# Optimization experiments

Hardware: AMD Instinct MI355X
Metric: run time of the kernel (lower is better)

The kernel has to match this reference:

```python
import jax, jax.numpy as jnp
import numpy as np

NPOINT = 1024   # number of sampled centers
NSAMPLE = 32    # neighbors per center
BN_EPS = 1e-5


def setup_inputs() -> dict:
    key = jax.random.key(0)
    ks = jax.random.split(key, 6)
    B, N, C = 8, 4096, 6
    inp = {
        "xyz": jax.random.normal(ks[0], (B, N, 3), jnp.float32),
        "points": jax.random.normal(ks[1], (B, N, C), jnp.float32),
        "W0": jax.random.normal(ks[2], (64, 9), jnp.float32) * 0.1,
        "g0": jnp.ones((64,), jnp.float32),
        "b0": jnp.zeros((64,), jnp.float32),
        "W1": jax.random.normal(ks[3], (64, 64), jnp.float32) * 0.1,
        "g1": jnp.ones((64,), jnp.float32),
        "b1": jnp.zeros((64,), jnp.float32),
        "W2": jax.random.normal(ks[4], (128, 64), jnp.float32) * 0.1,
        "g2": jnp.ones((128,), jnp.float32),
        "b2": jnp.zeros((128,), jnp.float32),
    }
    return inp


def sample_and_group(xyz, points):
    # xyz: [B,N,3], points: [B,N,C]
    B, N, _ = xyz.shape
    stride = N // NPOINT
    new_xyz = xyz[:, ::stride]                      # [B,S,3] deterministic subsample (FPS surrogate)
    # squared pairwise distances via ||a||^2 + ||b||^2 - 2 a.b  -> [B,S,N]
    d = (jnp.sum(new_xyz * new_xyz, -1)[:, :, None]
         + jnp.sum(xyz * xyz, -1)[:, None, :]
         - 2.0 * jnp.einsum('bsd,bnd->bsn', new_xyz, xyz))
    _, idx = jax.lax.top_k(-d, NSAMPLE)             # [B,S,K] KNN indices
    gather = jax.vmap(lambda arr, i: arr[i])        # per-batch gather: [N,C],[S,K] -> [S,K,C]
    g_xyz = gather(xyz, idx) - new_xyz[:, :, None, :]   # relative coords [B,S,K,3]
    g_pts = gather(points, idx)                     # [B,S,K,C]
    new_points = jnp.concatenate([g_xyz, g_pts], -1)    # [B,S,K,3+C]
    return new_xyz, new_points


def mlp_layer(x, W, g, b):
    # Conv2d(1x1, bias=False) == channel contraction; BN2d with batch stats; ReLU
    x = jnp.einsum('bskc,oc->bsko', x, W)
    m = jnp.mean(x, axis=(0, 1, 2))
    v = jnp.var(x, axis=(0, 1, 2))
    x = (x - m) * jax.lax.rsqrt(v + BN_EPS) * g + b
    return jax.nn.relu(x)


def reference(xyz, points, W0, g0, b0, W1, g1, b1, W2, g2, b2):
    new_xyz, x = sample_and_group(xyz, points)      # x: [B,S,K,9]
    x = mlp_layer(x, W0, g0, b0)
    x = mlp_layer(x, W1, g1, b1)
    x = mlp_layer(x, W2, g2, b2)
    new_points = jnp.max(x, axis=2)                 # max-pool over neighbor dim K -> [B,S,128]
    return new_xyz, new_points
```

## Files before the change

kernel.cpp:

```cpp
#include <hip/hip_runtime.h>
#include <float.h>
#include <stdint.h>

#define TOT   262144
#define NPTS  4096
#define KNN   32
#define BN_EPS 1e-5f
#define CAPV  64
#define TILEP 2048

typedef _Float16 f16;
typedef _Float16 f16x2 __attribute__((ext_vector_type(2)));
typedef _Float16 f16x4 __attribute__((ext_vector_type(4)));
typedef _Float16 f16x8 __attribute__((ext_vector_type(8)));
typedef float    f32x4 __attribute__((ext_vector_type(4)));

__device__ __forceinline__ int mbcnt64(unsigned long long m){
  return __builtin_amdgcn_mbcnt_hi((unsigned)(m>>32),
         __builtin_amdgcn_mbcnt_lo((unsigned)(m & 0xffffffffull), 0));
}
__device__ __forceinline__ unsigned f2ord(float f){
  unsigned u = __float_as_uint(f);
  return u ^ (((unsigned)((int)u >> 31)) | 0x80000000u);
}
__device__ __forceinline__ f16x2 bnrelu2(f16x2 x, f16x2 a, f16x2 c){
  f16x2 r = x*a + c;
  const f16 z = (f16)0.f;
  r[0] = r[0] > z ? r[0] : z;
  r[1] = r[1] > z ? r[1] : z;
  return r;
}
__device__ __forceinline__ void writeElem(int n, int e, float qx, float qy, float qz,
    const float* __restrict__ xb3, const float* __restrict__ fb,
    f16* __restrict__ grouped, f16* __restrict__ g16){
  float px = xb3[n*3+0], py = xb3[n*3+1], pz = xb3[n*3+2];
  f16 a[16];
  a[0]=(f16)(px-qx); a[1]=(f16)(py-qy); a[2]=(f16)(pz-qz);
  #pragma unroll
  for (int c6=0;c6<6;c6++) a[3+c6] = (f16)fb[n*6+c6];
  #pragma unroll
  for (int i=9;i<16;i++) a[i]=(f16)0.f;
  #pragma unroll
  for (int c=0;c<9;c++) grouped[c*TOT+e] = a[c];
  f16x8 lo, hi;
  #pragma unroll
  for (int i=0;i<8;i++){ lo[i]=a[i]; hi[i]=a[8+i]; }
  *(f16x8*)(g16 + (size_t)e*16)     = lo;
  *(f16x8*)(g16 + (size_t)e*16 + 8) = hi;
}

__global__ __launch_bounds__(256) void knn_gather(
    const float* __restrict__ xyz, const float* __restrict__ pts,
    f16* __restrict__ grouped, f16* __restrict__ g16,
    float* __restrict__ out_newxyz){
  __shared__ float4 tile[TILEP];
  __shared__ unsigned wk[8][CAPV];
  __shared__ unsigned short wi[8][CAPV];
  __shared__ unsigned lcnt[8];
  const int tid = threadIdx.x, lane = tid & 63, wv = tid >> 6;
  const int q0 = blockIdx.x*8 + wv*2;
  const int b  = (blockIdx.x*8) >> 10;
  const float* xb3 = xyz + (size_t)b*NPTS*3;
  float qx[2],qy[2],qz[2],qq[2];
  #pragma unroll
  for (int t=0;t<2;t++){
    int n = ((q0+t) & 1023)*4;
    qx[t]=xb3[n*3+0]; qy[t]=xb3[n*3+1]; qz[t]=xb3[n*3+2];
    qq[t]=qx[t]*qx[t]+qy[t]*qy[t]+qz[t]*qz[t];
  }
  if (tid < 8) lcnt[tid] = 0;
  if (lane == 0){
    #pragma unroll
    for (int t=0;t<2;t++){
      out_newxyz[(q0+t)*3+0]=qx[t]; out_newxyz[(q0+t)*3+1]=qy[t];
      out_newxyz[(q0+t)*3+2]=qz[t];
    }
  }

  float dmin[2] = {FLT_MAX, FLT_MAX};
  #pragma unroll 1
  for (int r=0; r<2; ++r){
    __syncthreads();
    #pragma unroll
    for (int k=0;k<8;k++){
      int p = r*TILEP + k*256 + tid;
      float x = xb3[p*3+0], y = xb3[p*3+1], z = xb3[p*3+2];
      tile[k*256+tid] = make_float4(x,y,z, x*x+y*y+z*z);
    }
    __syncthreads();
    #pragma unroll 4
    for (int i=0;i<32;i++){
      float4 P = tile[i*64+lane];
      #pragma unroll
      for (int t=0;t<2;t++){
        float d = (qq[t]+P.w) - 2.f*(qx[t]*P.x+qy[t]*P.y+qz[t]*P.z);
        dmin[t] = d < dmin[t] ? d : dmin[t];
      }
    }
  }
  float sm[2] = {dmin[0], dmin[1]};
  #pragma unroll
  for (int k=2;k<=64;k<<=1){
    #pragma unroll
    for (int j=k>>1;j>0;j>>=1){
      bool keepmin = (((lane&k)==0) == ((lane&j)==0));
      #pragma unroll
      for (int t=0;t<2;t++){
        float o = __shfl_xor(sm[t], j, 64);
        sm[t] = keepmin ? fminf(sm[t],o) : fmaxf(sm[t],o);
      }
    }
  }
  float Uf[2];
  #pragma unroll
  for (int t=0;t<2;t++) Uf[t] = __shfl(sm[t], 31, 64);

  #pragma unroll 1
  for (int r=0; r<2; ++r){
    __syncthreads();
    #pragma unroll
    for (int k=0;k<8;k++){
      int p = r*TILEP + k*256 + tid;
      float x = xb3[p*3+0], y = xb3[p*3+1], z = xb3[p*3+2];
      tile[k*256+tid] = make_float4(x,y,z, x*x+y*y+z*z);
    }
    __syncthreads();
    #pragma unroll 2
    for (int i=0;i<32;i++){
      float4 P = tile[i*64+lane];
      #pragma unroll
      for (int t=0;t<2;t++){
        float d = (qq[t]+P.w) - 2.f*(qx[t]*P.x+qy[t]*P.y+qz[t]*P.z);
        if (d <= Uf[t]){
          unsigned p2 = atomicAdd(&lcnt[wv*2+t], 1u);
          if (p2 < CAPV){
            wk[wv*2+t][p2] = f2ord(d);
            wi[wv*2+t][p2] = (unsigned short)(r*TILEP + i*64 + lane);
          }
        }
      }
    }
  }
  int cnt[2] = {(int)lcnt[wv*2], (int)lcnt[wv*2+1]};

  unsigned long long v[2];
  #pragma unroll
  for (int t=0;t<2;t++){
    unsigned myk = (lane<cnt[t]) ? wk[wv*2+t][lane] : 0xFFFFFFFFu;
    unsigned myi = (lane<cnt[t]) ? wi[wv*2+t][lane] : 0u;
    v[t] = (((unsigned long long)myk)<<16) | myi;
  }
  #pragma unroll
  for (int k=2;k<=64;k<<=1){
    #pragma unroll
    for (int j=k>>1;j>0;j>>=1){
      bool keepmin = (((lane&k)==0) == ((lane&j)==0));
      #pragma unroll
      for (int t=0;t<2;t++){
        unsigned long long o = __shfl_xor(v[t], j, 64);
        v[t] = keepmin ? (v[t]<o?v[t]:o) : (v[t]>o?v[t]:o);
      }
    }
  }

  const float* fb = pts + (size_t)b*NPTS*6;
  #pragma unroll 1
  for (int t=0;t<2;t++){
    const int ebase = (q0+t)*KNN;
    if (cnt[t] <= CAPV){
      if (lane < KNN){
        int n = (int)(v[t] & 0xffffull);
        writeElem(n, ebase+lane, qx[t],qy[t],qz[t], xb3, fb, grouped, g16);
      }
    } else {
      unsigned V=0;
      for (int bit=31; bit>=0; --bit){
        unsigned X = V | (1u<<bit);
        int c=0;
        for (int j=0;j<64;j++){
          int n = j*64+lane;
          float px=xb3[n*3], py=xb3[n*3+1], pz=xb3[n*3+2];
          float d = qq[t] + (px*px+py*py+pz*pz)
                  - 2.f*(qx[t]*px+qy[t]*py+qz[t]*pz);
          c += __popcll(__ballot(f2ord(d) < X));
        }
        if (c < KNN) V = X;
      }
      int cnt2=0;
      for (int pass=0; pass<2; ++pass){
        for (int j=0;j<64;j++){
          int n = j*64+lane;
          float px=xb3[n*3], py=xb3[n*3+1], pz=xb3[n*3+2];
          float d = qq[t] + (px*px+py*py+pz*pz)
                  - 2.f*(qx[t]*px+qy[t]*py+qz[t]*pz);
          unsigned kk = f2ord(d);
          bool sel = pass ? (kk==V) : (kk<V);
          unsigned long long msk = __ballot(sel);
          int pos = cnt2 + mbcnt64(msk);
          if (sel && pos < KNN)
            writeElem(n, ebase+pos, qx[t],qy[t],qz[t], xb3, fb, grouped, g16);
          cnt2 += __popcll(msk);
        }
      }
    }
  }
}

__global__ __launch_bounds__(256) void stats0m(const f16* __restrict__ grouped,
    float* __restrict__ s0m){
  const int lane = threadIdx.x & 63, wv = threadIdx.x >> 6;
  const int c = lane & 15, q = lane >> 4;
  const int base = (blockIdx.x*4 + wv)*512;
  f16x8 cfill = {};
  if (c == 9){
    #pragma unroll
    for (int i=0;i<8;i++) cfill[i] = (f16)1.f;
  }
  f32x4 acc = {0.f,0.f,0.f,0.f};
  #pragma unroll 4
  for (int chunk=0; chunk<16; ++chunk){
    int e = base + chunk*32 + q*8;
    f16x8 f = cfill;
    if (c < 9) f = *(const f16x8*)(grouped + (size_t)c*TOT + e);
    acc = __builtin_amdgcn_mfma_f32_16x16x32_f16(f, f, acc, 0,0,0);
  }
  __shared__ float red[4][16][16];
  #pragma unroll
  for (int i=0;i<4;i++) red[wv][q*4+i][c] = acc[i];
  __syncthreads();
  const int tid = threadIdx.x;
  if (tid < 160){
    int row = tid>>4, col = tid&15;
    float vv = red[0][row][col]+red[1][row][col]+red[2][row][col]+red[3][row][col];
    atomicAdd(&s0m[tid], vv);
  }
}

__device__ __forceinline__ void bn0_coeffs(int tid, const float* __restrict__ s0m,
    const float* __restrict__ W0, const float* __restrict__ g0,
    const float* __restrict__ b0, float* __restrict__ A0s,
    float* __restrict__ ac0c, float* __restrict__ Ssh){
  if (tid < 160) Ssh[tid] = s0m[tid];
  __syncthreads();
  if (tid < 64){
    float w[9];
    #pragma unroll
    for (int c=0;c<9;c++) w[c]=W0[tid*9+c];
    const float inv = 1.f/(float)TOT;
    float m=0.f;
    #pragma unroll
    for (int c=0;c<9;c++) m = fmaf(w[c], Ssh[c*16+9], m);
    m *= inv;
    float e2=0.f;
    #pragma unroll
    for (int c1=0;c1<9;c1++){
      float t=0.f;
      #pragma unroll
      for (int c2=0;c2<9;c2++) t = fmaf(w[c2], Ssh[c1*16+c2], t);
      e2 = fmaf(w[c1], t, e2);
    }
    e2 *= inv;
    float var = e2 - m*m;
    float a = g0[tid]*rsqrtf(var + BN_EPS);
    A0s[tid]  = a;
    ac0c[tid] = fmaf(-m, a, b0[tid]);
  }
  __syncthreads();
}

__global__ __launch_bounds__(256, 2) void layer1s(
    const f16* __restrict__ g16, const float* __restrict__ s0m,
    const float* __restrict__ W0, const float* __restrict__ g0,
    const float* __restrict__ b0, const float* __restrict__ W1,
    float* __restrict__ s1g){
  __shared__ f16 sW0[2048];
  __shared__ f16 sW1[4096];
  __shared__ float ac0c[64];
  __shared__ float A0s[64];
  __shared__ float Ssh[160];
  __shared__ f16 hb0[4][16][72];
  __shared__ float sred[4][128];
  const int tid = threadIdx.x;
  const int lane = tid & 63, wv = tid >> 6;
  const int e16 = lane & 15, q = lane >> 4;
  bn0_coeffs(tid, s0m, W0, g0, b0, A0s, ac0c, Ssh);
  #pragma unroll
  for (int idx=tid; idx<2048; idx+=256){
    int o = idx>>5, c = idx&31;
    sW0[idx] = (f16)(c<9 ? A0s[o]*W0[o*9+c] : 0.f);
  }
  #pragma unroll
  for (int idx=tid; idx<4096; idx+=256) sW1[idx] = (f16)W1[idx];
  __syncthreads();

  const int base = blockIdx.x*256 + wv*64;
  float ssum[16], ssq[16];
  #pragma unroll
  for (int i=0;i<16;i++){ ssum[i]=0.f; ssq[i]=0.f; }

  #pragma unroll 1
  for (int sub=0; sub<4; ++sub){
    int elem = base + sub*16 + e16;
    f16x8 bg = {};
    if (q < 2) bg = *(const f16x8*)(g16 + (size_t)elem*16 + q*8);
    #pragma unroll
    for (int m=0;m<4;m++){
      f32x4 acc = *(const f32x4*)(&ac0c[m*16 + q*4]);
      f16x8 A0f = *(const f16x8*)(&sW0[(m*16+e16)*32 + q*8]);
      acc = __builtin_amdgcn_mfma_f32_16x16x32_f16(A0f, bg, acc, 0,0,0);
      f16x4 w;
      w[0]=(f16)fmaxf(acc[0],0.f); w[1]=(f16)fmaxf(acc[1],0.f);
      w[2]=(f16)fmaxf(acc[2],0.f); w[3]=(f16)fmaxf(acc[3],0.f);
      *(f16x4*)(&hb0[wv][e16][m*16 + q*4]) = w;
    }
    f32x4 acc2[4];
    #pragma unroll
    for (int m=0;m<4;m++) acc2[m] = (f32x4){0.f,0.f,0.f,0.f};
    #pragma unroll
    for (int s=0;s<2;s++){
      f16x8 bh = *(const f16x8*)(&hb0[wv][e16][s*32 + q*8]);
      #pragma unroll
      for (int m=0;m<4;m++){
        f16x8 A1f = *(const f16x8*)(&sW1[(m*16+e16)*64 + s*32 + q*8]);
        acc2[m] = __builtin_amdgcn_mfma_f32_16x16x32_f16(A1f, bh, acc2[m], 0,0,0);
      }
    }
    #pragma unroll
    for (int m=0;m<4;m++)
      #pragma unroll
      for (int i=0;i<4;i++){
        float x = acc2[m][i];
        ssum[m*4+i] += x;
        ssq[m*4+i]  = fmaf(x, x, ssq[m*4+i]);
      }
  }
  #pragma unroll
  for (int t=0;t<16;t++){
    float a = ssum[t], bq = ssq[t];
    #pragma unroll
    for (int off=1; off<16; off<<=1){
      a  += __shfl_xor(a,  off, 64);
      bq += __shfl_xor(bq, off, 64);
    }
    ssum[t]=a; ssq[t]=bq;
  }
  if (e16==0){
    #pragma unroll
    for (int m=0;m<4;m++)
      #pragma unroll
      for (int i=0;i<4;i++){
        int ch = m*16 + q*4 + i;
        sred[wv][ch]    = ssum[m*4+i];
        sred[wv][64+ch] = ssq[m*4+i];
      }
  }
  __syncthreads();
  if (tid < 128){
    float v = sred[0][tid]+sred[1][tid]+sred[2][tid]+sred[3][tid];
    atomicAdd(&s1g[tid], v);
  }
}

__global__ __launch_bounds__(256, 2) void layer2max(
    const f16* __restrict__ g16, const float* __restrict__ s0m,
    const float* __restrict__ W0, const float* __restrict__ g0,
    const float* __restrict__ b0, const float* __restrict__ W1,
    const float* __restrict__ W2, const float* __restrict__ s1g,
    const float* __restrict__ g1, const float* __restrict__ b1,
    float* __restrict__ maxbuf, float* __restrict__ s2g){
  __shared__ f16 sW0[2048];
  __shared__ f16 sW1[4096];
  __shared__ float ac0c[64];
  __shared__ float A0s[64];
  __shared__ float Ssh[160];
  __shared__ f16 ac1s[128];
  __shared__ f16 hb0[4][16][72];
  __shared__ f16 hb1[4][2][16][72];
  float (*redbuf)[256] = (float(*)[256])hb0;
  const int tid = threadIdx.x;
  const int lane = tid & 63, wv = tid >> 6;
  const int e16 = lane & 15, q = lane >> 4;
  bn0_coeffs(tid, s0m, W0, g0, b0, A0s, ac0c, Ssh);
  #pragma unroll
  for (int idx=tid; idx<2048; idx+=256){
    int o = idx>>5, c = idx&31;
    sW0[idx] = (f16)(c<9 ? A0s[o]*W0[o*9+c] : 0.f);
  }
  #pragma unroll
  for (int idx=tid; idx<4096; idx+=256) sW1[idx] = (f16)W1[idx];
  if (tid < 64){
    const float inv = 1.f/(float)TOT;
    float m = s1g[tid]*inv;
    float vv = s1g[64+tid]*inv - m*m;
    float a = g1[tid]*rsqrtf(vv + BN_EPS);
    ac1s[tid]    = (f16)a;
    ac1s[64+tid] = (f16)fmaf(-m, a, b1[tid]);
  }
  __syncthreads();

  f16x8 Bw[8][2];
  #pragma unroll
  for (int nt=0;nt<8;nt++)
    #pragma unroll
    for (int s=0;s<2;s++){
      const float* src = W2 + (nt*16+e16)*64 + s*32 + q*8;
      f16x8 f;
      #pragma unroll
      for (int j=0;j<8;j++) f[j] = (f16)src[j];
      Bw[nt][s] = f;
    }

  float ssum[8], ssq[8];
  #pragma unroll
  for (int i=0;i<8;i++){ ssum[i]=0.f; ssq[i]=0.f; }

  #pragma unroll 1
  for (int qq=0; qq<2; ++qq){
    const int qid = blockIdx.x*8 + wv*2 + qq;
    #pragma unroll 1
    for (int mt=0; mt<2; ++mt){
      int elem = qid*32 + mt*16 + e16;
      f16x8 bg = {};
      if (q < 2) bg = *(const f16x8*)(g16 + (size_t)elem*16 + q*8);
      #pragma unroll
      for (int m=0;m<4;m++){
        f32x4 acc = *(const f32x4*)(&ac0c[m*16 + q*4]);
        f16x8 A0f = *(const f16x8*)(&sW0[(m*16+e16)*32 + q*8]);
        acc = __builtin_amdgcn_mfma_f32_16x16x32_f16(A0f, bg, acc, 0,0,0);
        f16x4 w;
        w[0]=(f16)fmaxf(acc[0],0.f); w[1]=(f16)fmaxf(acc[1],0.f);
        w[2]=(f16)fmaxf(acc[2],0.f); w[3]=(f16)fmaxf(acc[3],0.f);
        *(f16x4*)(&hb0[wv][e16][m*16 + q*4]) = w;
      }
      f32x4 acc2[4];
      #pragma unroll
      for (int m=0;m<4;m++) acc2[m] = (f32x4){0.f,0.f,0.f,0.f};
      #pragma unroll
      for (int s=0;s<2;s++){
        f16x8 bh = *(const f16x8*)(&hb0[wv][e16][s*32 + q*8]);
        #pragma unroll
        for (int m=0;m<4;m++){
          f16x8 A1f = *(const f16x8*)(&sW1[(m*16+e16)*64 + s*32 + q*8]);
          acc2[m] = __builtin_amdgcn_mfma_f32_16x16x32_f16(A1f, bh, acc2[m], 0,0,0);
        }
      }
      #pragma unroll
      for (int m=0;m<4;m++){
        f16x4 a4 = *(const f16x4*)(&ac1s[m*16 + q*4]);
        f16x4 c4 = *(const f16x4*)(&ac1s[64 + m*16 + q*4]);
        f16x2 p0 = bnrelu2((f16x2){(f16)acc2[m][0], (f16)acc2[m][1]},
                           (f16x2){a4[0],a4[1]}, (f16x2){c4[0],c4[1]});
        f16x2 p1 = bnrelu2((f16x2){(f16)acc2[m][2], (f16)acc2[m][3]},
                           (f16x2){a4[2],a4[3]}, (f16x2){c4[2],c4[3]});
        f16x4 w; w[0]=p0[0]; w[1]=p0[1]; w[2]=p1[0]; w[3]=p1[1];
        *(f16x4*)(&hb1[wv][mt][e16][m*16 + q*4]) = w;
      }
    }
    float mx[8];
    #pragma unroll
    for (int g=0; g<2; ++g){
      f32x4 acc3[4][2];
      #pragma unroll
      for (int j=0;j<4;j++){ acc3[j][0]=(f32x4){0,0,0,0}; acc3[j][1]=(f32x4){0,0,0,0}; }
      #pragma unroll
      for (int mt=0; mt<2; ++mt)
        #pragma unroll
        for (int s=0;s<2;s++){
          f16x8 af = *(const f16x8*)(&hb1[wv][mt][e16][s*32 + q*8]);
          #pragma unroll
          for (int j=0;j<4;j++)
            acc3[j][mt] = __builtin_amdgcn_mfma_f32_16x16x32_f16(af, Bw[g*4+j][s], acc3[j][mt], 0,0,0);
        }
      #pragma unroll
      for (int j=0;j<4;j++){
        int nt = g*4 + j;
        f32x4 u = acc3[j][0], vv = acc3[j][1];
        float m1 = fmaxf(fmaxf(u[0],u[1]), fmaxf(u[2],u[3]));
        float m2 = fmaxf(fmaxf(vv[0],vv[1]), fmaxf(vv[2],vv[3]));
        float m = fmaxf(m1, m2);
        ssum[nt] += (u[0]+u[1])+(u[2]+u[3]) + (vv[0]+vv[1])+(vv[2]+vv[3]);
        float sq = 0.f;
        #pragma unroll
        for (int i=0;i<4;i++){ sq = fmaf(u[i],u[i],sq); sq = fmaf(vv[i],vv[i],sq); }
        ssq[nt] += sq;
        m = fmaxf(m, __shfl_xor(m, 16, 64));
        m = fmaxf(m, __shfl_xor(m, 32, 64));
        mx[nt] = m;
      }
    }
    if (lane < 16){
      #pragma unroll
      for (int nt=0;nt<8;nt++) maxbuf[(size_t)qid*128 + nt*16 + lane] = mx[nt];
    }
  }
  #pragma unroll
  for (int nt=0;nt<8;nt++){
    ssum[nt] += __shfl_xor(ssum[nt], 16, 64);
    ssum[nt] += __shfl_xor(ssum[nt], 32, 64);
    ssq[nt]  += __shfl_xor(ssq[nt], 16, 64);
    ssq[nt]  += __shfl_xor(ssq[nt], 32, 64);
  }
  __syncthreads();
  if (q==0){
    #pragma unroll
    for (int nt=0;nt<8;nt++){
      redbuf[wv][nt*16+e16]     = ssum[nt];
      redbuf[wv][128+nt*16+e16] = ssq[nt];
    }
  }
  __syncthreads();
  float v = redbuf[0][tid]+redbuf[1][tid]+redbuf[2][tid]+redbuf[3][tid];
  atomicAdd(&s2g[tid], v);
}

__global__ __launch_bounds__(256) void apply2(
    const float4* __restrict__ maxbuf4, const float* __restrict__ s2g,
    const float* __restrict__ g2, const float* __restrict__ b2,
    float4* __restrict__ outp4){
  __shared__ float a2s[128], c2s[128];
  const int tid = threadIdx.x;
  if (tid < 128){
    const float inv = 1.f/(float)TOT;
    float m = s2g[tid]*inv;
    float v = s2g[128+tid]*inv - m*m;
    float a = g2[tid]*rsqrtf(v + BN_EPS);
    a2s[tid] = a;
    c2s[tid] = fmaf(-m, a, b2[tid]);
  }
  __syncthreads();
  int i = blockIdx.x*256 + tid;
  int c4 = (i & 31)*4;
  float4 m = maxbuf4[i];
  float4 r;
  r.x = fmaxf(fmaf(m.x, a2s[c4+0], c2s[c4+0]), 0.f);
  r.y = fmaxf(fmaf(m.y, a2s[c4+1], c2s[c4+1]), 0.f);
  r.z = fmaxf(fmaf(m.z, a2s[c4+2], c2s[c4+2]), 0.f);
  r.w = fmaxf(fmaf(m.w, a2s[c4+3], c2s[c4+3]), 0.f);
  outp4[i] = r;
}

extern "C" void kernel_launch(void* const* d_in, const int* in_sizes, int n_in,
                              void* d_out, int out_size, void* d_ws, size_t ws_size,
                              hipStream_t stream){
  const float* xyz = (const float*)d_in[0];
  const float* pts = (const float*)d_in[1];
  const float* W0  = (const float*)d_in[2];
  const float* g0  = (const float*)d_in[3];
  const float* b0  = (const float*)d_in[4];
  const float* W1  = (const float*)d_in[5];
  const float* g1  = (const float*)d_in[6];
  const float* b1  = (const float*)d_in[7];
  const float* W2  = (const float*)d_in[8];
  const float* g2  = (const float*)d_in[9];
  const float* b2  = (const float*)d_in[10];
  float* out = (float*)d_out;

  float* ws      = (float*)d_ws;
  f16*   grouped = (f16*)ws;
  f16*   g16     = (f16*)(ws + (size_t)5*TOT);
  float* maxbuf  = ws + (size_t)13*TOT;
  float* s0m     = ws + (size_t)17*TOT;
  float* s1g     = s0m + 160;
  float* s2g     = s1g + 128;

  (void)hipMemsetAsync(s0m, 0, 544*sizeof(float), stream);
  knn_gather<<<1024, 256, 0, stream>>>(xyz, pts, grouped, g16, out);
  stats0m   <<< 128, 256, 0, stream>>>(grouped, s0m);
  layer1s   <<<1024, 256, 0, stream>>>(g16, s0m, W0, g0, b0, W1, s1g);
  layer2max <<<1024, 256, 0, stream>>>(g16, s0m, W0, g0, b0, W1, W2, s1g, g1, b1, maxbuf, s2g);
  apply2    <<<1024, 256, 0, stream>>>((const float4*)maxbuf, s2g, g2, b2, (float4*)(out + 24576));
}
```

Before: 202.4 us.

## Store layer-1 pre-BN activations in fp16 instead of recomputing layers 0-1

layer1s now writes its pre-BN layer-1 outputs to a new fp16 workspace buffer (262144x64). layer2max reads these back, applies the BN1+ReLU affine, and runs only the layer-2 MFMAs, so it no longer recomputes layer 0 and layer 1 or stages weights and intermediates in shared memory. This trades recomputation and LDS traffic for about 32 MB of extra global write and read. The layer-2 accumulators are also restructured to hold all 8 output tiles at once.

```diff
diff --git a/kernel.cpp b/kernel.cpp
--- a/kernel.cpp
+++ b/kernel.cpp
@@ -272,7 +272,7 @@
     const f16* __restrict__ g16, const float* __restrict__ s0m,
     const float* __restrict__ W0, const float* __restrict__ g0,
     const float* __restrict__ b0, const float* __restrict__ W1,
-    float* __restrict__ s1g){
+    f16* __restrict__ x1h, float* __restrict__ s1g){
   __shared__ f16 sW0[2048];
   __shared__ f16 sW1[4096];
   __shared__ float ac0c[64];
@@ -326,13 +326,17 @@
       }
     }
     #pragma unroll
-    for (int m=0;m<4;m++)
+    for (int m=0;m<4;m++){
+      f16x4 w;
       #pragma unroll
       for (int i=0;i<4;i++){
         float x = acc2[m][i];
         ssum[m*4+i] += x;
         ssq[m*4+i]  = fmaf(x, x, ssq[m*4+i]);
-      }
+        w[i] = (f16)x;
+      }
+      *(f16x4*)(x1h + (size_t)elem*64 + m*16 + q*4) = w;
+    }
   }
   #pragma unroll
   for (int t=0;t<16;t++){
@@ -362,32 +366,15 @@
 }
 
 __global__ __launch_bounds__(256, 2) void layer2max(
-    const f16* __restrict__ g16, const float* __restrict__ s0m,
-    const float* __restrict__ W0, const float* __restrict__ g0,
-    const float* __restrict__ b0, const float* __restrict__ W1,
-    const float* __restrict__ W2, const float* __restrict__ s1g,
-    const float* __restrict__ g1, const float* __restrict__ b1,
+    const f16* __restrict__ x1h, const float* __restrict__ W2,
+    const float* __restrict__ s1g, const float* __restrict__ g1,
+    const float* __restrict__ b1,
     float* __restrict__ maxbuf, float* __restrict__ s2g){
-  __shared__ f16 sW0[2048];
-  __shared__ f16 sW1[4096];
-  __shared__ float ac0c[64];
-  __shared__ float A0s[64];
-  __shared__ float Ssh[160];
   __shared__ f16 ac1s[128];
-  __shared__ f16 hb0[4][16][72];
-  __shared__ f16 hb1[4][2][16][72];
-  float (*redbuf)[256] = (float(*)[256])hb0;
+  __shared__ float lds[4][256];
   const int tid = threadIdx.x;
   const int lane = tid & 63, wv = tid >> 6;
   const int e16 = lane & 15, q = lane >> 4;
-  bn0_coeffs(tid, s0m, W0, g0, b0, A0s, ac0c, Ssh);
-  #pragma unroll
-  for (int idx=tid; idx<2048; idx+=256){
-    int o = idx>>5, c = idx&31;
-    sW0[idx] = (f16)(c<9 ? A0s[o]*W0[o*9+c] : 0.f);
-  }
-  #pragma unroll
-  for (int idx=tid; idx<4096; idx+=256) sW1[idx] = (f16)W1[idx];
   if (tid < 64){
     const float inv = 1.f/(float)TOT;
     float m = s1g[tid]*inv;
@@ -409,6 +396,14 @@
       for (int j=0;j<8;j++) f[j] = (f16)src[j];
       Bw[nt][s] = f;
     }
+  f16x2 a1p[2][4], c1p[2][4];
+  #pragma unroll
+  for (int s=0;s<2;s++)
+    #pragma unroll
+    for (int j2=0;j2<4;j2++){
+      a1p[s][j2] = ((const f16x2*)ac1s)[s*16 + q*4 + j2];
+      c1p[s][j2] = ((const f16x2*)(ac1s+64))[s*16 + q*4 + j2];
+    }
 
   float ssum[8], ssq[8];
   #pragma unroll
@@ -417,76 +412,38 @@
   #pragma unroll 1
   for (int qq=0; qq<2; ++qq){
     const int qid = blockIdx.x*8 + wv*2 + qq;
-    #pragma unroll 1
+    f32x4 acc3[8][2];
+    #pragma unroll
+    for (int nt=0;nt<8;nt++){ acc3[nt][0]=(f32x4){0,0,0,0}; acc3[nt][1]=(f32x4){0,0,0,0}; }
+    #pragma unroll
     for (int mt=0; mt<2; ++mt){
-      int elem = qid*32 + mt*16 + e16;
-      f16x8 bg = {};
-      if (q < 2) bg = *(const f16x8*)(g16 + (size_t)elem*16 + q*8);
-      #pragma unroll
-      for (int m=0;m<4;m++){
-        f32x4 acc = *(const f32x4*)(&ac0c[m*16 + q*4]);
-        f16x8 A0f = *(const f16x8*)(&sW0[(m*16+e16)*32 + q*8]);
-        acc = __builtin_amdgcn_mfma_f32_16x16x32_f16(A0f, bg, acc, 0,0,0);
-        f16x4 w;
-        w[0]=(f16)fmaxf(acc[0],0.f); w[1]=(f16)fmaxf(acc[1],0.f);
-        w[2]=(f16)fmaxf(acc[2],0.f); w[3]=(f16)fmaxf(acc[3],0.f);
-        *(f16x4*)(&hb0[wv][e16][m*16 + q*4]) = w;
-      }
-      f32x4 acc2[4];
-      #pragma unroll
-      for (int m=0;m<4;m++) acc2[m] = (f32x4){0.f,0.f,0.f,0.f};
+      const f16* rowp = x1h + (size_t)(qid*32 + mt*16 + e16)*64;
       #pragma unroll
       for (int s=0;s<2;s++){
-        f16x8 bh = *(const f16x8*)(&hb0[wv][e16][s*32 + q*8]);
+        f16x8 a = *(const f16x8*)(rowp + s*32 + q*8);
+        f16x2* a2 = (f16x2*)&a;
         #pragma unroll
-        for (int m=0;m<4;m++){
-          f16x8 A1f = *(const f16x8*)(&sW1[(m*16+e16)*64 + s*32 + q*8]);
-          acc2[m] = __builtin_amdgcn_mfma_f32_16x16x32_f16(A1f, bh, acc2[m], 0,0,0);
-        }
-      }
-      #pragma unroll
-      for (int m=0;m<4;m++){
-        f16x4 a4 = *(const f16x4*)(&ac1s[m*16 + q*4]);
-        f16x4 c4 = *(const f16x4*)(&ac1s[64 + m*16 + q*4]);
-        f16x2 p0 = bnrelu2((f16x2){(f16)acc2[m][0], (f16)acc2[m][1]},
-                           (f16x2){a4[0],a4[1]}, (f16x2){c4[0],c4[1]});
-        f16x2 p1 = bnrelu2((f16x2){(f16)acc2[m][2], (f16)acc2[m][3]},
-                           (f16x2){a4[2],a4[3]}, (f16x2){c4[2],c4[3]});
-        f16x4 w; w[0]=p0[0]; w[1]=p0[1]; w[2]=p1[0]; w[3]=p1[1];
-        *(f16x4*)(&hb1[wv][mt][e16][m*16 + q*4]) = w;
+        for (int j2=0;j2<4;j2++) a2[j2] = bnrelu2(a2[j2], a1p[s][j2], c1p[s][j2]);
+        #pragma unroll
+        for (int nt=0;nt<8;nt++)
+          acc3[nt][mt] = __builtin_amdgcn_mfma_f32_16x16x32_f16(a, Bw[nt][s], acc3[nt][mt], 0,0,0);
       }
     }
     float mx[8];
     #pragma unroll
-    for (int g=0; g<2; ++g){
-      f32x4 acc3[4][2];
-      #pragma unroll
-      for (int j=0;j<4;j++){ acc3[j][0]=(f32x4){0,0,0,0}; acc3[j][1]=(f32x4){0,0,0,0}; }
-      #pragma unroll
-      for (int mt=0; mt<2; ++mt)
-        #pragma unroll
-        for (int s=0;s<2;s++){
-          f16x8 af = *(const f16x8*)(&hb1[wv][mt][e16][s*32 + q*8]);
-          #pragma unroll
-          for (int j=0;j<4;j++)
-            acc3[j][mt] = __builtin_amdgcn_mfma_f32_16x16x32_f16(af, Bw[g*4+j][s], acc3[j][mt], 0,0,0);
-        }
-      #pragma unroll
-      for (int j=0;j<4;j++){
-        int nt = g*4 + j;
-        f32x4 u = acc3[j][0], vv = acc3[j][1];
-        float m1 = fmaxf(fmaxf(u[0],u[1]), fmaxf(u[2],u[3]));
-        float m2 = fmaxf(fmaxf(vv[0],vv[1]), fmaxf(vv[2],vv[3]));
-        float m = fmaxf(m1, m2);
-        ssum[nt] += (u[0]+u[1])+(u[2]+u[3]) + (vv[0]+vv[1])+(vv[2]+vv[3]);
-        float sq = 0.f;
-        #pragma unroll
-        for (int i=0;i<4;i++){ sq = fmaf(u[i],u[i],sq); sq = fmaf(vv[i],vv[i],sq); }
-        ssq[nt] += sq;
-        m = fmaxf(m, __shfl_xor(m, 16, 64));
-        m = fmaxf(m, __shfl_xor(m, 32, 64));
-        mx[nt] = m;
-      }
+    for (int nt=0;nt<8;nt++){
+      f32x4 u = acc3[nt][0], vv = acc3[nt][1];
+      float m1 = fmaxf(fmaxf(u[0],u[1]), fmaxf(u[2],u[3]));
+      float m2 = fmaxf(fmaxf(vv[0],vv[1]), fmaxf(vv[2],vv[3]));
+      float m = fmaxf(m1, m2);
+      ssum[nt] += (u[0]+u[1])+(u[2]+u[3]) + (vv[0]+vv[1])+(vv[2]+vv[3]);
+      float sq = 0.f;
+      #pragma unroll
+      for (int i=0;i<4;i++){ sq = fmaf(u[i],u[i],sq); sq = fmaf(vv[i],vv[i],sq); }
+      ssq[nt] += sq;
+      m = fmaxf(m, __shfl_xor(m, 16, 64));
+      m = fmaxf(m, __shfl_xor(m, 32, 64));
+      mx[nt] = m;
     }
     if (lane < 16){
       #pragma unroll
@@ -500,16 +457,15 @@
     ssq[nt]  += __shfl_xor(ssq[nt], 16, 64);
     ssq[nt]  += __shfl_xor(ssq[nt], 32, 64);
   }
-  __syncthreads();
   if (q==0){
     #pragma unroll
     for (int nt=0;nt<8;nt++){
-      redbuf[wv][nt*16+e16]     = ssum[nt];
-      redbuf[wv][128+nt*16+e16] = ssq[nt];
-    }
-  }
-  __syncthreads();
-  float v = redbuf[0][tid]+redbuf[1][tid]+redbuf[2][tid]+redbuf[3][tid];
+      lds[wv][nt*16+e16]     = ssum[nt];
+      lds[wv][128+nt*16+e16] = ssq[nt];
+    }
+  }
+  __syncthreads();
+  float v = lds[0][tid]+lds[1][tid]+lds[2][tid]+lds[3][tid];
   atomicAdd(&s2g[tid], v);
 }
 
@@ -559,14 +515,15 @@
   f16*   grouped = (f16*)ws;
   f16*   g16     = (f16*)(ws + (size_t)5*TOT);
   float* maxbuf  = ws + (size_t)13*TOT;
-  float* s0m     = ws + (size_t)17*TOT;
+  f16*   x1h     = (f16*)(ws + (size_t)17*TOT);
+  float* s0m     = ws + (size_t)49*TOT;
   float* s1g     = s0m + 160;
   float* s2g     = s1g + 128;
 
   (void)hipMemsetAsync(s0m, 0, 544*sizeof(float), stream);
   knn_gather<<<1024, 256, 0, stream>>>(xyz, pts, grouped, g16, out);
   stats0m   <<< 128, 256, 0, stream>>>(grouped, s0m);
-  layer1s   <<<1024, 256, 0, stream>>>(g16, s0m, W0, g0, b0, W1, s1g);
-  layer2max <<<1024, 256, 0, stream>>>(g16, s0m, W0, g0, b0, W1, W2, s1g, g1, b1, maxbuf, s2g);
+  layer1s   <<<1024, 256, 0, stream>>>(g16, s0m, W0, g0, b0, W1, x1h, s1g);
+  layer2max <<<1024, 256, 0, stream>>>(x1h, W2, s1g, g1, b1, maxbuf, s2g);
   apply2    <<<1024, 256, 0, stream>>>((const float4*)maxbuf, s2g, g2, b2, (float4*)(out + 24576));
 }
```

Result: no change. 206.4 us (+2.0%).
